# Performance work log

Hardware: AMD Instinct MI355X
Metric: run time of the kernel (lower is better)

Reference implementation:

```python
import jax, jax.numpy as jnp
import numpy as np

L = 18                      # tree depth, N = 2**L - 1 nodes (complete binary tree)
N = 2**L - 1               # 262143
D = 128                     # embedding dim
V = 100000                  # vocab size of the single data type
E = 8                       # edge_count


def setup_inputs() -> dict:
    key = jax.random.key(0)
    ks = jax.random.split(key, 8)
    data = jax.random.randint(ks[0], (N,), 0, V)
    edges = jax.random.randint(ks[1], (N,), 0, E)
    data_vecs = jax.random.normal(ks[2], (V, D), dtype=jnp.float32) * 0.1
    # torch uses torch.rand (U[0,1)); scaled for numerical stability over 18 levels
    data_W = jax.random.uniform(ks[3], (D, D), dtype=jnp.float32) * 0.1
    data_b = jax.random.uniform(ks[4], (D,), dtype=jnp.float32) * 0.1
    edge_W = jax.random.uniform(ks[5], (E, D, D), dtype=jnp.float32) * (2.0 / D)
    edge_b = jax.random.uniform(ks[6], (E, D), dtype=jnp.float32) * 0.1
    score_W = jax.random.uniform(ks[7], (D, 1), dtype=jnp.float32)
    return {"data": data, "edges": edges, "data_vecs": data_vecs,
            "data_W": data_W, "data_b": data_b, "edge_W": edge_W,
            "edge_b": edge_b, "score_W": score_W}


def reference(data, edges, data_vecs, data_W, data_b, edge_W, edge_b, score_W):
    # per-node leaf term: addmm(data_bias, data_vecs[data], data_W)  -> [N, D]
    raw = data_vecs[data] @ data_W + data_b
    ret = raw    # value returned to the parent (leaves: unclamped)
    emb = raw    # stored embedding (internal nodes: pre-clamp h)
    # bottom-up over levels; level l occupies indices [2**l - 1, 2**(l+1) - 1)
    for l in reversed(range(L - 1)):
        p0, npar = 2**l - 1, 2**l
        c0, M = 2**(l + 1) - 1, 2**(l + 1)
        child_ret = ret[c0:c0 + M]              # [M, D], siblings adjacent
        eids = edges[c0:c0 + M]                 # [M]
        # edge-weighted child transform: child @ edge_W[e] + edge_b[e]
        contrib = edge_b[eids]
        for e in range(E):                      # small static edge loop
            contrib = contrib + jnp.where((eids == e)[:, None], child_ret, 0.0) @ edge_W[e]
        # sum the two children of each parent, then (leaf + children) / (nc + 1)
        contrib = contrib.reshape(npar, 2, D).sum(axis=1)
        h = (raw[p0:p0 + npar] + contrib) / 3.0
        emb = emb.at[p0:p0 + npar].set(h)
        ret = ret.at[p0:p0 + npar].set(jnp.maximum(h, 0.0))
    scores = (emb @ score_W)[:, 0]              # [N]
    return scores


if __name__ == "__main__":
    out = reference(**setup_inputs())
    print(out.shape, out.dtype)
```

## Files before the change

### kernel.cpp

```cpp
#include <hip/hip_runtime.h>

#define D 128
#define NLVL 17
#define TS 64
#define LVLPAD 1024
#define LDSTR 136
#define LEAF_BLKS 2057
#define CHUNK 2048
#define CNT_BLKS 128
#define PLVL0 10
#define CBASE 2047
#define NBINS 56

typedef float  floatx4 __attribute__((ext_vector_type(4)));
typedef short  shortx8 __attribute__((ext_vector_type(8)));

__device__ __forceinline__ unsigned short f2bf(float f) {
    unsigned u = __float_as_uint(f);
    u += 0x7FFFu + ((u >> 16) & 1u);
    return (unsigned short)(u >> 16);
}
__device__ __forceinline__ float bf2f(unsigned short h) {
    return __uint_as_float(((unsigned)h) << 16);
}
__device__ __forceinline__ int lvl_base_dev(int l) { return ((2 << l) - 2) + LVLPAD * l; }

__global__ __launch_bounds__(256) void prep_kernel(
    const float* __restrict__ dW, const float* __restrict__ db,
    const float* __restrict__ eW, const float* __restrict__ eb,
    const float* __restrict__ sWs, const float* __restrict__ vecs,
    const int* __restrict__ edges,
    unsigned short* __restrict__ ewt, unsigned short* __restrict__ cwt,
    unsigned short* __restrict__ dwt, float* __restrict__ dcomp,
    float* __restrict__ sv, float* __restrict__ s0, int* __restrict__ ctr,
    int* __restrict__ gcnt128, int Nn,
    unsigned short* __restrict__ vbf, int n4)
{
    __shared__ float smem[8448];
    const int b = blockIdx.x, t = threadIdx.x;
    if (b < 32) {
        float* w_s = smem;
        float* cs  = smem + 4096;
        const int e = b >> 2, cc = b & 3;
        for (int i = t; i < D * 8; i += 256) {
            const int k = i >> 3, j4 = i & 7;
            ((float4*)w_s)[i] = ((const float4*)eW)[((size_t)e * D + k) * 32 + cc * 8 + j4];
        }
        __syncthreads();
        const int r2 = t >> 1, h = t & 1;
        float4 acc[4];
        #pragma unroll
        for (int m = 0; m < 4; m++) acc[m] = make_float4(0.f, 0.f, 0.f, 0.f);
        for (int k = 0; k < D; k++) {
            const float a = dW[(size_t)r2 * D + k];
            #pragma unroll
            for (int m = 0; m < 4; m++) {
                const float4 w4 = ((const float4*)w_s)[k * 8 + h * 4 + m];
                acc[m].x += a * w4.x; acc[m].y += a * w4.y; acc[m].z += a * w4.z; acc[m].w += a * w4.w;
            }
        }
        #pragma unroll
        for (int m = 0; m < 4; m++) {
            cs[r2 * 33 + h * 16 + m * 4 + 0] = acc[m].x;
            cs[r2 * 33 + h * 16 + m * 4 + 1] = acc[m].y;
            cs[r2 * 33 + h * 16 + m * 4 + 2] = acc[m].z;
            cs[r2 * 33 + h * 16 + m * 4 + 3] = acc[m].w;
        }
        __syncthreads();
        {
            const int nn = t >> 3, kseg = t & 7, k0 = kseg * 16;
            unsigned ow[8];
            #pragma unroll
            for (int i2 = 0; i2 < 8; i2++) {
                const unsigned short lo = f2bf(cs[(k0 + 2 * i2) * 33 + nn]);
                const unsigned short hi = f2bf(cs[(k0 + 2 * i2 + 1) * 33 + nn]);
                ow[i2] = (unsigned)lo | ((unsigned)hi << 16);
            }
            uint4* dstp = (uint4*)(cwt + (size_t)e * D * D + (size_t)(cc * 32 + nn) * D + k0);
            dstp[0] = make_uint4(ow[0], ow[1], ow[2], ow[3]);
            dstp[1] = make_uint4(ow[4], ow[5], ow[6], ow[7]);
        }
        if (t < 32) {
            float a2 = 0.f;
            for (int k = 0; k < D; k++) a2 += db[k] * w_s[k * 32 + t];
            dcomp[e * D + cc * 32 + t] = a2 + eb[e * D + cc * 32 + t];
        }
    } else if (b < 41) {
        float* lds = smem;
        const int bb = b - 32;
        const float* src = (bb < 8) ? (eW + (size_t)bb * D * D) : dW;
        unsigned short* dst = (bb < 8) ? (ewt + (size_t)bb * D * D) : dwt;
        for (int half = 0; half < 2; half++) {
            __syncthreads();
            for (int i = t; i < 64 * D / 4; i += 256) {
                float4 v = ((const float4*)src)[half * (64 * D / 4) + i];
                const int k = (i * 4) >> 7, n = (i * 4) & 127;
                lds[k * 129 + n]     = v.x;
                lds[k * 129 + n + 1] = v.y;
                lds[k * 129 + n + 2] = v.z;
                lds[k * 129 + n + 3] = v.w;
            }
            __syncthreads();
            const int n = t >> 1, hh = t & 1;
            for (int kk = 0; kk < 32; kk++) {
                const int k = hh * 32 + kk;
                dst[(size_t)n * D + half * 64 + k] = f2bf(lds[k * 129 + n]);
            }
        }
    } else if (b == 41) {
        float* red = smem;
        if (t < NBINS) ctr[t] = 0;
        if (t < D) {
            float acc = 0.f;
            for (int j = 0; j < D; j++) acc += dW[(size_t)t * D + j] * sWs[j];
            sv[t] = acc;
        }
        red[t] = (t < D) ? db[t] * sWs[t] : 0.f;
        __syncthreads();
        for (int s = 128; s > 0; s >>= 1) { if (t < s) red[t] += red[t + s]; __syncthreads(); }
        if (t == 0) s0[0] = red[0];
    } else if (b < 42 + CNT_BLKS) {
        int* lc = (int*)smem;
        if (t < NBINS) lc[t] = 0;
        __syncthreads();
        for (int c = CBASE + (b - 42) * 256 + t; c < Nn; c += CNT_BLKS * 256) {
            const int e = edges[c];
            const int p = (c - 1) >> 1;
            const int l = 31 - __clz(p + 1);
            atomicAdd(&lc[(l - PLVL0) * 8 + e], 1);
        }
        __syncthreads();
        if (t < NBINS) gcnt128[(b - 42) * NBINS + t] = lc[t];
    } else {
        for (int i = (b - 42 - CNT_BLKS) * 256 + t; i < n4; i += (gridDim.x - 42 - CNT_BLKS) * 256) {
            const float4 v = ((const float4*)vecs)[i];
            uint2 o;
            o.x = (unsigned)f2bf(v.x) | ((unsigned)f2bf(v.y) << 16);
            o.y = (unsigned)f2bf(v.z) | ((unsigned)f2bf(v.w) << 16);
            ((uint2*)vbf)[i] = o;
        }
    }
}

__global__ __launch_bounds__(256) void place_kernel(
    const int* __restrict__ edges, const int* __restrict__ gcnt128,
    int* __restrict__ gstart, int* __restrict__ glim,
    int* __restrict__ ctr, int* __restrict__ perm, int Nn)
{
    __shared__ unsigned char key_s[CHUNK];
    __shared__ int part[256];
    __shared__ int tot[NBINS];
    __shared__ int lcnt[NBINS], lbase[NBINS];
    __shared__ int gs_s[7 * 9], gl_s[7 * 8];
    const int t = threadIdx.x;
    {
        const int k = t & 63, bs = t >> 6;
        int s = 0;
        if (k < NBINS)
            for (int bb = bs; bb < CNT_BLKS; bb += 4) s += gcnt128[bb * NBINS + k];
        part[t] = s;
    }
    if (t < NBINS) lcnt[t] = 0;
    __syncthreads();
    if (t < NBINS)
        tot[t] = part[t] + part[t + 64] + part[t + 128] + part[t + 192];
    __syncthreads();
    if (t == 0) {
        for (int li = 0; li < 7; li++) {
            int acc = 0;
            for (int e = 0; e < 8; e++) {
                gs_s[li * 9 + e] = acc;
                gl_s[li * 8 + e] = acc + tot[li * 8 + e];
                acc = (acc + tot[li * 8 + e] + (TS - 1)) & ~(TS - 1);
            }
            gs_s[li * 9 + 8] = acc;
        }
    }
    __syncthreads();
    if (blockIdx.x == 0) {
        if (t < 63) gstart[PLVL0 * 9 + t] = gs_s[t];
        if (t < NBINS) glim[PLVL0 * 8 + t] = gl_s[t];
    }
    const int base = CBASE + blockIdx.x * CHUNK;
    for (int i = t; i < CHUNK; i += 256) {
        const int c = base + i;
        if (c < Nn) {
            const int e = edges[c];
            const int p = (c - 1) >> 1;
            const int l = 31 - __clz(p + 1);
            const int kk = (l - PLVL0) * 8 + e;
            key_s[i] = (unsigned char)kk;
            atomicAdd(&lcnt[kk], 1);
        } else key_s[i] = 255;
    }
    __syncthreads();
    if (t < NBINS) {
        const int n = lcnt[t];
        lbase[t] = n ? atomicAdd(&ctr[t], n) : 0;
        lcnt[t] = 0;
    }
    __syncthreads();
    for (int i = t; i < CHUNK; i += 256) {
        const int c = base + i;
        if (c >= Nn) continue;
        const int kk = key_s[i];
        if (kk == 255) continue;
        const int off = atomicAdd(&lcnt[kk], 1);
        const int l = (kk >> 3) + PLVL0, e = kk & 7;
        const int pos = gs_s[(l - PLVL0) * 9 + e] + lbase[kk] + off;
        perm[lvl_base_dev(l) + pos] = c;
    }
}

__global__ __launch_bounds__(256, 6) void leaf_embed_kernel(
    unsigned short* __restrict__ X,
    const unsigned short* __restrict__ vbf,
    const int* __restrict__ data,
    const int* __restrict__ perm,
    const int* __restrict__ gstart9,
    const int* __restrict__ glim8,
    const unsigned short* __restrict__ cwt,
    const float* __restrict__ dcomp,
    const float* __restrict__ sv, const float* __restrict__ s0p,
    const unsigned short* __restrict__ dwt,
    const float* __restrict__ db,
    float* __restrict__ out,
    int NI, int lbase_leaf)
{
    __shared__ unsigned short a_s[TS * LDSTR];
    const int t = threadIdx.x;
    const bool is_leaf = (blockIdx.x < LEAF_BLKS);
    const int r = t >> 2, h4 = t & 3;

    int e = 0, c;
    const unsigned short* Wg;
    const float* bias;
    if (is_leaf) {
        const int ts = blockIdx.x * TS;
        if (ts >= gstart9[8]) return;
        #pragma unroll
        for (int j = 1; j < 8; j++) if (ts >= gstart9[j]) e = j;
        const int p = ts + r;
        c = (p < glim8[e]) ? perm[lbase_leaf + p] : -1;
        Wg = cwt + (size_t)e * D * D;
        bias = dcomp + (size_t)e * D;
    } else {
        const int node = (blockIdx.x - LEAF_BLKS) * TS + r;
        c = (node < NI) ? node : -1;
        Wg = dwt;
        bias = db;
    }

    {
        unsigned short* dst = a_s + r * LDSTR + h4 * 32;
        if (c >= 0) {
            const uint4* src = (const uint4*)(vbf + (size_t)data[c] * D + h4 * 32);
            if (is_leaf) {
                float sc = 0.f;
                #pragma unroll
                for (int j = 0; j < 4; j++) {
                    const uint4 v = src[j];
                    const unsigned* pv = (const unsigned*)&v;
                    #pragma unroll
                    for (int u = 0; u < 4; u++) {
                        const int n = h4 * 32 + j * 8 + u * 2;
                        sc += bf2f((unsigned short)pv[u]) * sv[n]
                            + bf2f((unsigned short)(pv[u] >> 16)) * sv[n + 1];
                    }
                    ((uint4*)dst)[j] = v;
                }
                sc += __shfl_xor(sc, 1, 64);
                sc += __shfl_xor(sc, 2, 64);
                if (h4 == 0) out[c] = sc + s0p[0];
            } else {
                #pragma unroll
                for (int j = 0; j < 4; j++) ((uint4*)dst)[j] = src[j];
            }
        } else {
            #pragma unroll
            for (int j = 0; j < 4; j++) ((uint4*)dst)[j] = make_uint4(0u, 0u, 0u, 0u);
        }
    }
    __syncthreads();

    const int lane = t & 63, wv = t >> 6;
    const int cq = lane & 15, q = lane >> 4;
    const floatx4 z4 = {0.f, 0.f, 0.f, 0.f};
    floatx4 acc[4][2];
    #pragma unroll
    for (int i = 0; i < 4; i++) { acc[i][0] = z4; acc[i][1] = z4; }
    #pragma unroll
    for (int ks = 0; ks < 4; ks++) {
        shortx8 bfr[2];
        #pragma unroll
        for (int nl = 0; nl < 2; nl++) {
            const int n = (wv * 2 + nl) * 16 + cq;
            bfr[nl] = *(const shortx8*)(Wg + (size_t)n * D + ks * 32 + q * 8);
        }
        #pragma unroll
        for (int mt = 0; mt < 4; mt++) {
            const shortx8 af = *(const shortx8*)(a_s + (mt * 16 + cq) * LDSTR + ks * 32 + q * 8);
            acc[mt][0] = __builtin_amdgcn_mfma_f32_16x16x32_bf16(bfr[0], af, acc[mt][0], 0, 0, 0);
            acc[mt][1] = __builtin_amdgcn_mfma_f32_16x16x32_bf16(bfr[1], af, acc[mt][1], 0, 0, 0);
        }
    }
    __syncthreads();
    #pragma unroll
    for (int nl = 0; nl < 2; nl++) {
        const int n0 = (wv * 2 + nl) * 16 + q * 4;
        const float4 b4 = *(const float4*)(bias + n0);
        #pragma unroll
        for (int mt = 0; mt < 4; mt++) {
            const int m = mt * 16 + cq;
            const unsigned lo = (unsigned)f2bf(acc[mt][nl][0] + b4.x)
                              | ((unsigned)f2bf(acc[mt][nl][1] + b4.y) << 16);
            const unsigned hi = (unsigned)f2bf(acc[mt][nl][2] + b4.z)
                              | ((unsigned)f2bf(acc[mt][nl][3] + b4.w) << 16);
            *(uint2*)(a_s + (size_t)m * LDSTR + n0) = make_uint2(lo, hi);
        }
    }
    __syncthreads();
    if (c >= 0) {
        uint4* dstg = (uint4*)(X + (size_t)c * D + h4 * 32);
        const uint4* srcl = (const uint4*)(a_s + r * LDSTR + h4 * 32);
        #pragma unroll
        for (int j = 0; j < 4; j++) dstg[j] = srcl[j];
    }
}

__global__ __launch_bounds__(256, 6) void tree_gemm_kernel(
    unsigned short* __restrict__ X,
    const int* __restrict__ perm,
    const int* __restrict__ gstart9,
    const int* __restrict__ glim8,
    const unsigned short* __restrict__ ewt,
    const float* __restrict__ eb,
    const float* __restrict__ svec,
    float* __restrict__ out,
    int lbase)
{
    __shared__ unsigned short a_s[TS * LDSTR];
    const int t = threadIdx.x;
    const int ts = blockIdx.x * TS;
    if (ts >= gstart9[8]) return;
    int e = 0;
    #pragma unroll
    for (int j = 1; j < 8; j++) if (ts >= gstart9[j]) e = j;
    const int r = t >> 2, h4 = t & 3;
    const int p = ts + r;
    const int c = (p < glim8[e]) ? perm[lbase + p] : -1;
    const unsigned short* Wg = ewt + (size_t)e * D * D;

    {
        unsigned short* dst = a_s + r * LDSTR + h4 * 32;
        if (c >= 0) {
            const uint4* xr = (const uint4*)(X + (size_t)c * D + h4 * 32);
            const uint4* ya = (const uint4*)(X + (size_t)(2 * c + 1) * D + h4 * 32);
            const uint4* yb = (const uint4*)(X + (size_t)(2 * c + 2) * D + h4 * 32);
            const float inv3 = 1.0f / 3.0f;
            float sc = 0.f;
            #pragma unroll
            for (int j = 0; j < 4; j++) {
                uint4 ra = xr[j], rb = ya[j], rc = yb[j];
                const unsigned* pa = (const unsigned*)&ra;
                const unsigned* pb = (const unsigned*)&rb;
                const unsigned* pc = (const unsigned*)&rc;
                unsigned ou[4];
                #pragma unroll
                for (int u = 0; u < 4; u++) {
                    const float h0 = (bf2f((unsigned short)pa[u]) + bf2f((unsigned short)pb[u])
                                    + bf2f((unsigned short)pc[u])) * inv3;
                    const float h1 = (bf2f((unsigned short)(pa[u] >> 16)) + bf2f((unsigned short)(pb[u] >> 16))
                                    + bf2f((unsigned short)(pc[u] >> 16))) * inv3;
                    const int n = h4 * 32 + j * 8 + u * 2;
                    sc += h0 * svec[n] + h1 * svec[n + 1];
                    unsigned short q0 = f2bf(h0), q1 = f2bf(h1);
                    q0 = (q0 & 0x8000u) ? 0 : q0;
                    q1 = (q1 & 0x8000u) ? 0 : q1;
                    ou[u] = (unsigned)q0 | ((unsigned)q1 << 16);
                }
                ((uint4*)dst)[j] = make_uint4(ou[0], ou[1], ou[2], ou[3]);
            }
            sc += __shfl_xor(sc, 1, 64);
            sc += __shfl_xor(sc, 2, 64);
            if (h4 == 0) out[c] = sc;
        } else {
            #pragma unroll
            for (int j = 0; j < 4; j++) ((uint4*)dst)[j] = make_uint4(0u, 0u, 0u, 0u);
        }
    }
    __syncthreads();
    const int lane = t & 63, wv = t >> 6;
    const int cq = lane & 15, q = lane >> 4;
    const floatx4 z4 = {0.f, 0.f, 0.f, 0.f};
    floatx4 acc[4][2];
    #pragma unroll
    for (int i = 0; i < 4; i++) { acc[i][0] = z4; acc[i][1] = z4; }
    #pragma unroll
    for (int ks = 0; ks < 4; ks++) {
        shortx8 bfr[2];
        #pragma unroll
        for (int nl = 0; nl < 2; nl++) {
            const int n = (wv * 2 + nl) * 16 + cq;
            bfr[nl] = *(const shortx8*)(Wg + (size_t)n * D + ks * 32 + q * 8);
        }
        #pragma unroll
        for (int mt = 0; mt < 4; mt++) {
            const shortx8 af = *(const shortx8*)(a_s + (mt * 16 + cq) * LDSTR + ks * 32 + q * 8);
            acc[mt][0] = __builtin_amdgcn_mfma_f32_16x16x32_bf16(bfr[0], af, acc[mt][0], 0, 0, 0);
            acc[mt][1] = __builtin_amdgcn_mfma_f32_16x16x32_bf16(bfr[1], af, acc[mt][1], 0, 0, 0);
        }
    }
    __syncthreads();
    #pragma unroll
    for (int nl = 0; nl < 2; nl++) {
        const int n0 = (wv * 2 + nl) * 16 + q * 4;
        const float4 b4 = *(const float4*)(eb + (size_t)e * D + n0);
        #pragma unroll
        for (int mt = 0; mt < 4; mt++) {
            const int m = mt * 16 + cq;
            const unsigned lo = (unsigned)f2bf(acc[mt][nl][0] + b4.x)
                              | ((unsigned)f2bf(acc[mt][nl][1] + b4.y) << 16);
            const unsigned hi = (unsigned)f2bf(acc[mt][nl][2] + b4.z)
                              | ((unsigned)f2bf(acc[mt][nl][3] + b4.w) << 16);
            *(uint2*)(a_s + (size_t)m * LDSTR + n0) = make_uint2(lo, hi);
        }
    }
    __syncthreads();
    if (c >= 0) {
        uint4* dstg = (uint4*)(X + (size_t)c * D + h4 * 32);
        const uint4* srcl = (const uint4*)(a_s + r * LDSTR + h4 * 32);
        #pragma unroll
        for (int j = 0; j < 4; j++) dstg[j] = srcl[j];
    }
}

__global__ __launch_bounds__(256) void sub_kernel(
    unsigned short* __restrict__ X,
    const float* __restrict__ eW,
    const float* __restrict__ eb,
    const int* __restrict__ edges,
    const float* __restrict__ sW,
    float* __restrict__ out,
    int rbase, int nlev)
{
    __shared__ __align__(16) float xbuf[4][D];
    const int t = threadIdx.x, wv = t >> 6, lane = t & 63;
    const int u = rbase + blockIdx.x;
    const int j2 = lane * 2;
    const float inv3 = 1.0f / 3.0f;

    for (int lev = nlev - 1; lev >= 0; lev--) {
        const int first = ((u + 1) << lev) - 1;
        const int cnt = 1 << lev;
        for (int i = wv; i < cnt; i += 4) {
            const int n = first + i;
            const unsigned ra = *(const unsigned*)(X + (size_t)n * D + j2);
            const unsigned rb = *(const unsigned*)(X + (size_t)(2 * n + 1) * D + j2);
            const unsigned rc = *(const unsigned*)(X + (size_t)(2 * n + 2) * D + j2);
            const float h0 = (bf2f((unsigned short)ra) + bf2f((unsigned short)rb)
                            + bf2f((unsigned short)rc)) * inv3;
            const float h1 = (bf2f((unsigned short)(ra >> 16)) + bf2f((unsigned short)(rb >> 16))
                            + bf2f((unsigned short)(rc >> 16))) * inv3;
            float sc = h0 * sW[j2] + h1 * sW[j2 + 1];
            #pragma unroll
            for (int o = 32; o > 0; o >>= 1) sc += __shfl_xor(sc, o, 64);
            if (lane == 0) out[n] = sc;
            if (n == 0) continue;
            float2 x2 = make_float2(fmaxf(h0, 0.f), fmaxf(h1, 0.f));
            *(float2*)(xbuf[wv] + j2) = x2;
            const int e = edges[n];
            const float* W = eW + (size_t)e * D * D;
            float y0 = 0.f, y1 = 0.f;
            #pragma unroll 8
            for (int k4 = 0; k4 < 32; k4++) {
                const float4 xk = *(const float4*)(xbuf[wv] + k4 * 4);
                const float2 w0 = *(const float2*)(W + (size_t)(k4 * 4 + 0) * D + j2);
                const float2 w1 = *(const float2*)(W + (size_t)(k4 * 4 + 1) * D + j2);
                const float2 w2 = *(const float2*)(W + (size_t)(k4 * 4 + 2) * D + j2);
                const float2 w3 = *(const float2*)(W + (size_t)(k4 * 4 + 3) * D + j2);
                y0 += xk.x * w0.x + xk.y * w1.x + xk.z * w2.x + xk.w * w3.x;
                y1 += xk.x * w0.y + xk.y * w1.y + xk.z * w2.y + xk.w * w3.y;
            }
            y0 += eb[e * D + j2];
            y1 += eb[e * D + j2 + 1];
            const unsigned o = (unsigned)f2bf(y0) | ((unsigned)f2bf(y1) << 16);
            *(unsigned*)(X + (size_t)n * D + j2) = o;
        }
        __syncthreads();
    }
}

extern "C" void kernel_launch(void* const* d_in, const int* in_sizes, int n_in,
                              void* d_out, int out_size, void* d_ws, size_t ws_size,
                              hipStream_t stream) {
    const int*   data      = (const int*)d_in[0];
    const int*   edges     = (const int*)d_in[1];
    const float* data_vecs = (const float*)d_in[2];
    const float* data_W    = (const float*)d_in[3];
    const float* data_b    = (const float*)d_in[4];
    const float* edge_W    = (const float*)d_in[5];
    const float* edge_b    = (const float*)d_in[6];
    const float* score_W   = (const float*)d_in[7];
    float* out = (float*)d_out;

    const int Nn = in_sizes[0];
    const int NI = Nn >> 1;
    const int VD = in_sizes[2];
    const int PERM_TOTAL = (Nn - 1) + LVLPAD * NLVL;

    char* w = (char*)d_ws;
    size_t off = 0;
    unsigned short* X = (unsigned short*)(w + off); off += (size_t)Nn * D * 2;
    int* perm = (int*)(w + off);  off += (size_t)PERM_TOTAL * 4;
    off = (off + 255) & ~(size_t)255;
    int* gstart  = (int*)(w + off); off += NLVL * 9 * 4;
    int* glim    = (int*)(w + off); off += NLVL * 8 * 4;
    int* gcnt128 = (int*)(w + off); off += CNT_BLKS * 64 * 4;
    int* ctr     = (int*)(w + off); off += 64 * 4;
    off = (off + 255) & ~(size_t)255;
    float* dcomp = (float*)(w + off); off += 8 * D * 4;
    float* sv    = (float*)(w + off); off += D * 4;
    float* s0    = (float*)(w + off); off += 256;
    off = (off + 255) & ~(size_t)255;
    unsigned short* ewt = (unsigned short*)(w + off); off += (size_t)8 * D * D * 2;
    unsigned short* cwt = (unsigned short*)(w + off); off += (size_t)8 * D * D * 2;
    unsigned short* dwt = (unsigned short*)(w + off); off += (size_t)D * D * 2;
    off = (off + 255) & ~(size_t)255;
    unsigned short* vbf = (unsigned short*)(w + off); off += (size_t)VD * 2;

    prep_kernel<<<42 + CNT_BLKS + 1024, 256, 0, stream>>>(
        data_W, data_b, edge_W, edge_b, score_W, data_vecs, edges,
        ewt, cwt, dwt, dcomp, sv, s0, ctr, gcnt128, Nn, vbf, VD / 4);

    const int place_blks = (Nn - CBASE + CHUNK - 1) / CHUNK;
    place_kernel<<<place_blks, 256, 0, stream>>>(edges, gcnt128, gstart, glim, ctr, perm, Nn);

    {
        const int embed_blks = (NI + TS - 1) / TS;
        const int lbase_leaf = ((2 << 16) - 2) + LVLPAD * 16;
        leaf_embed_kernel<<<LEAF_BLKS + embed_blks, 256, 0, stream>>>(
            X, vbf, data, perm, gstart + 16 * 9, glim + 16 * 8,
            cwt, dcomp, sv, s0, dwt, data_b, out, NI, lbase_leaf);
    }

    for (int l = 15; l >= PLVL0; l--) {
        const int M = 2 << l;
        const int lbase = ((2 << l) - 2) + LVLPAD * l;
        tree_gemm_kernel<<<M / TS + 8, 256, 0, stream>>>(
            X, perm, gstart + l * 9, glim + l * 8, ewt, edge_b, score_W, out, lbase);
    }

    sub_kernel<<<128, 256, 0, stream>>>(X, edge_W, edge_b, edges, score_W, out, 127, 4);
    sub_kernel<<<8, 256, 0, stream>>>(X, edge_W, edge_b, edges, score_W, out, 7, 4);
    sub_kernel<<<1, 256, 0, stream>>>(X, edge_W, edge_b, edges, score_W, out, 0, 3);
}
```

Measured before the change: 294.9 us.

## Fuse internal-node data embedding GEMM into per-level tree kernel

```diff
diff --git a/kernel.cpp b/kernel.cpp
--- a/kernel.cpp
+++ b/kernel.cpp
@@ -11,6 +11,7 @@
 #define PLVL0 10
 #define CBASE 2047
 #define NBINS 56
+#define NRAW 2047
 
 typedef float  floatx4 __attribute__((ext_vector_type(4)));
 typedef short  shortx8 __attribute__((ext_vector_type(8)));
@@ -328,11 +329,15 @@
     }
 }
 
-__global__ __launch_bounds__(256, 6) void tree_gemm_kernel(
+__global__ __launch_bounds__(256, 3) void tree_fused_kernel(
     unsigned short* __restrict__ X,
+    const unsigned short* __restrict__ vbf,
+    const int* __restrict__ data,
     const int* __restrict__ perm,
     const int* __restrict__ gstart9,
     const int* __restrict__ glim8,
+    const unsigned short* __restrict__ dwt,
+    const float* __restrict__ db,
     const unsigned short* __restrict__ ewt,
     const float* __restrict__ eb,
     const float* __restrict__ svec,
@@ -340,6 +345,8 @@
     int lbase)
 {
     __shared__ unsigned short a_s[TS * LDSTR];
+    __shared__ float cs_s[TS][132];
+    __shared__ float scorebuf[TS];
     const int t = threadIdx.x;
     const int ts = blockIdx.x * TS;
     if (ts >= gstart9[8]) return;
@@ -349,51 +356,104 @@
     const int r = t >> 2, h4 = t & 3;
     const int p = ts + r;
     const int c = (p < glim8[e]) ? perm[lbase + p] : -1;
-    const unsigned short* Wg = ewt + (size_t)e * D * D;
-
+
+    if (t < TS) scorebuf[t] = 0.f;
     {
         unsigned short* dst = a_s + r * LDSTR + h4 * 32;
+        float* cd = &cs_s[r][h4 * 32];
         if (c >= 0) {
-            const uint4* xr = (const uint4*)(X + (size_t)c * D + h4 * 32);
+            const uint4* src = (const uint4*)(vbf + (size_t)data[c] * D + h4 * 32);
             const uint4* ya = (const uint4*)(X + (size_t)(2 * c + 1) * D + h4 * 32);
             const uint4* yb = (const uint4*)(X + (size_t)(2 * c + 2) * D + h4 * 32);
-            const float inv3 = 1.0f / 3.0f;
-            float sc = 0.f;
             #pragma unroll
             for (int j = 0; j < 4; j++) {
-                uint4 ra = xr[j], rb = ya[j], rc = yb[j];
-                const unsigned* pa = (const unsigned*)&ra;
+                ((uint4*)dst)[j] = src[j];
+                const uint4 rb = ya[j], rc = yb[j];
                 const unsigned* pb = (const unsigned*)&rb;
                 const unsigned* pc = (const unsigned*)&rc;
-                unsigned ou[4];
                 #pragma unroll
                 for (int u = 0; u < 4; u++) {
-                    const float h0 = (bf2f((unsigned short)pa[u]) + bf2f((unsigned short)pb[u])
-                                    + bf2f((unsigned short)pc[u])) * inv3;
-                    const float h1 = (bf2f((unsigned short)(pa[u] >> 16)) + bf2f((unsigned short)(pb[u] >> 16))
-                                    + bf2f((unsigned short)(pc[u] >> 16))) * inv3;
-                    const int n = h4 * 32 + j * 8 + u * 2;
-                    sc += h0 * svec[n] + h1 * svec[n + 1];
-                    unsigned short q0 = f2bf(h0), q1 = f2bf(h1);
-                    q0 = (q0 & 0x8000u) ? 0 : q0;
-                    q1 = (q1 & 0x8000u) ? 0 : q1;
-                    ou[u] = (unsigned)q0 | ((unsigned)q1 << 16);
+                    cd[j * 8 + u * 2]     = bf2f((unsigned short)pb[u]) + bf2f((unsigned short)pc[u]);
+                    cd[j * 8 + u * 2 + 1] = bf2f((unsigned short)(pb[u] >> 16)) + bf2f((unsigned short)(pc[u] >> 16));
                 }
-                ((uint4*)dst)[j] = make_uint4(ou[0], ou[1], ou[2], ou[3]);
-            }
-            sc += __shfl_xor(sc, 1, 64);
-            sc += __shfl_xor(sc, 2, 64);
-            if (h4 == 0) out[c] = sc;
+            }
         } else {
             #pragma unroll
-            for (int j = 0; j < 4; j++) ((uint4*)dst)[j] = make_uint4(0u, 0u, 0u, 0u);
-        }
-    }
-    __syncthreads();
+            for (int j = 0; j < 4; j++) {
+                ((uint4*)dst)[j] = make_uint4(0u, 0u, 0u, 0u);
+                ((float4*)cd)[j * 2]     = make_float4(0.f, 0.f, 0.f, 0.f);
+                ((float4*)cd)[j * 2 + 1] = make_float4(0.f, 0.f, 0.f, 0.f);
+            }
+        }
+    }
+    __syncthreads();
+
     const int lane = t & 63, wv = t >> 6;
     const int cq = lane & 15, q = lane >> 4;
     const floatx4 z4 = {0.f, 0.f, 0.f, 0.f};
     floatx4 acc[4][2];
+    #pragma unroll
+    for (int i = 0; i < 4; i++) { acc[i][0] = z4; acc[i][1] = z4; }
+    #pragma unroll
+    for (int ks = 0; ks < 4; ks++) {
+        shortx8 bfr[2];
+        #pragma unroll
+        for (int nl = 0; nl < 2; nl++) {
+            const int n = (wv * 2 + nl) * 16 + cq;
+            bfr[nl] = *(const shortx8*)(dwt + (size_t)n * D + ks * 32 + q * 8);
+        }
+        #pragma unroll
+        for (int mt = 0; mt < 4; mt++) {
+            const shortx8 af = *(const shortx8*)(a_s + (mt * 16 + cq) * LDSTR + ks * 32 + q * 8);
+            acc[mt][0] = __builtin_amdgcn_mfma_f32_16x16x32_bf16(bfr[0], af, acc[mt][0], 0, 0, 0);
+            acc[mt][1] = __builtin_amdgcn_mfma_f32_16x16x32_bf16(bfr[1], af, acc[mt][1], 0, 0, 0);
+        }
+    }
+    const float inv3 = 1.0f / 3.0f;
+    float sp[4] = {0.f, 0.f, 0.f, 0.f};
+    uint2 hpk[2][4];
+    #pragma unroll
+    for (int nl = 0; nl < 2; nl++) {
+        const int n0 = (wv * 2 + nl) * 16 + q * 4;
+        const float4 db4 = *(const float4*)(db + n0);
+        const float4 sv4 = *(const float4*)(svec + n0);
+        #pragma unroll
+        for (int mt = 0; mt < 4; mt++) {
+            const int m = mt * 16 + cq;
+            const float4 cs4 = *(const float4*)(&cs_s[m][n0]);
+            const float h0 = (acc[mt][nl][0] + db4.x + cs4.x) * inv3;
+            const float h1 = (acc[mt][nl][1] + db4.y + cs4.y) * inv3;
+            const float h2 = (acc[mt][nl][2] + db4.z + cs4.z) * inv3;
+            const float h3 = (acc[mt][nl][3] + db4.w + cs4.w) * inv3;
+            sp[mt] += h0 * sv4.x + h1 * sv4.y + h2 * sv4.z + h3 * sv4.w;
+            unsigned short q0 = f2bf(h0), q1 = f2bf(h1), q2 = f2bf(h2), q3 = f2bf(h3);
+            q0 = (q0 & 0x8000u) ? 0 : q0;
+            q1 = (q1 & 0x8000u) ? 0 : q1;
+            q2 = (q2 & 0x8000u) ? 0 : q2;
+            q3 = (q3 & 0x8000u) ? 0 : q3;
+            hpk[nl][mt] = make_uint2((unsigned)q0 | ((unsigned)q1 << 16),
+                                     (unsigned)q2 | ((unsigned)q3 << 16));
+        }
+    }
+    #pragma unroll
+    for (int mt = 0; mt < 4; mt++) {
+        sp[mt] += __shfl_xor(sp[mt], 16, 64);
+        sp[mt] += __shfl_xor(sp[mt], 32, 64);
+    }
+    __syncthreads();
+    #pragma unroll
+    for (int nl = 0; nl < 2; nl++) {
+        const int n0 = (wv * 2 + nl) * 16 + q * 4;
+        #pragma unroll
+        for (int mt = 0; mt < 4; mt++)
+            *(uint2*)(a_s + (size_t)(mt * 16 + cq) * LDSTR + n0) = hpk[nl][mt];
+    }
+    if (q == 0) {
+        #pragma unroll
+        for (int mt = 0; mt < 4; mt++) atomicAdd(&scorebuf[mt * 16 + cq], sp[mt]);
+    }
+    __syncthreads();
+    const unsigned short* Wg = ewt + (size_t)e * D * D;
     #pragma unroll
     for (int i = 0; i < 4; i++) { acc[i][0] = z4; acc[i][1] = z4; }
     #pragma unroll
@@ -432,6 +492,7 @@
         const uint4* srcl = (const uint4*)(a_s + r * LDSTR + h4 * 32);
         #pragma unroll
         for (int j = 0; j < 4; j++) dstg[j] = srcl[j];
+        if (h4 == 1) out[c] = scorebuf[r];
     }
 }
 
@@ -505,7 +566,6 @@
     float* out = (float*)d_out;
 
     const int Nn = in_sizes[0];
-    const int NI = Nn >> 1;
     const int VD = in_sizes[2];
     const int PERM_TOTAL = (Nn - 1) + LVLPAD * NLVL;
 
@@ -537,18 +597,19 @@
     place_kernel<<<place_blks, 256, 0, stream>>>(edges, gcnt128, gstart, glim, ctr, perm, Nn);
 
     {
-        const int embed_blks = (NI + TS - 1) / TS;
+        const int embed_blks = (NRAW + TS - 1) / TS;
         const int lbase_leaf = ((2 << 16) - 2) + LVLPAD * 16;
         leaf_embed_kernel<<<LEAF_BLKS + embed_blks, 256, 0, stream>>>(
             X, vbf, data, perm, gstart + 16 * 9, glim + 16 * 8,
-            cwt, dcomp, sv, s0, dwt, data_b, out, NI, lbase_leaf);
+            cwt, dcomp, sv, s0, dwt, data_b, out, NRAW, lbase_leaf);
     }
 
     for (int l = 15; l >= PLVL0; l--) {
         const int M = 2 << l;
         const int lbase = ((2 << l) - 2) + LVLPAD * l;
-        tree_gemm_kernel<<<M / TS + 8, 256, 0, stream>>>(
-            X, perm, gstart + l * 9, glim + l * 8, ewt, edge_b, score_W, out, lbase);
+        tree_fused_kernel<<<M / TS + 8, 256, 0, stream>>>(
+            X, vbf, data, perm, gstart + l * 9, glim + l * 8,
+            dwt, data_b, ewt, edge_b, score_W, out, lbase);
     }
 
     sub_kernel<<<128, 256, 0, stream>>>(X, edge_W, edge_b, edges, score_W, out, 127, 4);
```

New measurement: 283.4 us. -3.9%, faster.
